# Optimization experiments

Measured on AMD Instinct MI355X. Metric: run time of the kernel, lower is better.

## Reference

```python
import jax, jax.numpy as jnp
import numpy as np

N, E, DIM, A = 100_000, 1_600_000, 128, 5
ODE_STEPS = 5


def setup_inputs() -> dict:
    key = jax.random.key(0)
    ks = jax.random.split(key, 10)
    s = np.float32(1.0 / np.sqrt(DIM))
    s2 = np.float32(1.0 / np.sqrt(2 * DIM))
    return dict(
        x=jax.random.normal(ks[0], (N, DIM), jnp.float32),
        edge_index=jax.random.randint(ks[1], (2, E), 0, N, dtype=jnp.int32),
        node_anchor=jax.random.normal(ks[2], (A, DIM), jnp.float32) * s,
        W_att=jax.random.normal(ks[3], (A, DIM), jnp.float32) * s,
        b_att=jnp.zeros((A,), jnp.float32),
        edge_anchor=jax.random.normal(ks[4], (A, DIM), jnp.float32) * s,
        W_edge=jax.random.normal(ks[5], (A, 2 * DIM), jnp.float32) * s2,
        b_edge=jnp.zeros((A,), jnp.float32),
        W1=jax.random.normal(ks[6], (DIM, 2 * DIM), jnp.float32) * s2,
        b1=jnp.zeros((DIM,), jnp.float32),
        W2=jax.random.normal(ks[7], (DIM, DIM), jnp.float32) * s,
        b2=jnp.zeros((DIM,), jnp.float32),
    )


def reference(x, edge_index, node_anchor, W_att, b_att, edge_anchor,
              W_edge, b_edge, W1, b1, W2, b2):
    src, dst = edge_index[0], edge_index[1]

    # NodePromptplus.add: attention-weighted anchor prompt added to x
    att = jax.nn.softmax(x @ W_att.T + b_att, axis=1)          # [N, A]
    node_x = x + att @ node_anchor                             # [N, DIM]

    # EdgePromptplus.get_prompt: per-edge prompt from endpoint features
    combined_x = jnp.concatenate([x[src], x[dst]], axis=1)     # [E, 2*DIM]
    b = jax.nn.softmax(jax.nn.leaky_relu(combined_x @ W_edge.T + b_edge), axis=1)  # [E, A]
    edge_prompt = b @ edge_anchor                              # [E, DIM]

    # index_add_ scatter to both endpoints
    agg = jnp.zeros_like(x).at[src].add(edge_prompt).at[dst].add(edge_prompt)

    # Euler ODE integration: dx = W2 @ relu(W1 @ [evolved, agg])
    dt = jnp.float32(1.0 / ODE_STEPS)
    W1a, W1b = W1[:, :DIM], W1[:, DIM:]
    agg_proj = agg @ W1b.T + b1   # constant across steps; hoisted out of loop
    ev = node_x
    for _ in range(ODE_STEPS):
        h = jax.nn.relu(ev @ W1a.T + agg_proj)
        ev = ev + dt * (h @ W2.T + b2)
    return ev, edge_prompt
```

## Files before the change

kernel.cpp:

```cpp
#include <hip/hip_runtime.h>

#define NN 100000
#define NE 1600000
#define DIM 128
#define NA 5
#define STEPS 5

#define CSCALE3 128.0f
#define CINV3   0.0078125f

typedef float f32x4 __attribute__((ext_vector_type(4)));
typedef short short8v __attribute__((ext_vector_type(8)));
typedef unsigned u32x4 __attribute__((ext_vector_type(4)));

__device__ __forceinline__ float wsum(float v) {
#pragma unroll
  for (int off = 32; off > 0; off >>= 1) v += __shfl_xor(v, off, 64);
  return v;
}

__device__ __forceinline__ unsigned pkhi(float a, float b) {
  return __builtin_amdgcn_perm(__float_as_uint(b), __float_as_uint(a),
                               0x07060302u);
}
__device__ __forceinline__ float lof(float x) {
  return x - __uint_as_float(__float_as_uint(x) & 0xffff0000u);
}
__device__ __forceinline__ float upk0(unsigned u) {
  return __uint_as_float(u << 16);
}
__device__ __forceinline__ float upk1(unsigned u) {
  return __uint_as_float(u & 0xffff0000u);
}

__global__ __launch_bounds__(128) void k_prepM(
    const float* __restrict__ W1, const float* __restrict__ edge_anchor,
    float* __restrict__ M) {
  const int i = threadIdx.x;
  const int a = blockIdx.x;
  float s = 0.f;
  for (int j = 0; j < DIM; ++j)
    s = fmaf(edge_anchor[a * DIM + j], W1[i * 2 * DIM + DIM + j], s);
  M[a * DIM + i] = s;
}

__global__ __launch_bounds__(256) void k_wpack(
    const float* __restrict__ W1, const float* __restrict__ W2,
    uint4* __restrict__ wp) {
  const int mat = blockIdx.x >> 3, nf = blockIdx.x & 7;
  const int ks = threadIdx.x >> 6, lane = threadIdx.x & 63;
  const int g = lane >> 4, r = lane & 15;
  float v[8];
  if (mat == 0) {
    const float* src = W1 + (16 * nf + r) * 256 + 32 * ks + 8 * g;
    float4 a = *(const float4*)src;
    float4 b = *(const float4*)(src + 4);
    v[0] = a.x; v[1] = a.y; v[2] = a.z; v[3] = a.w;
    v[4] = b.x; v[5] = b.y; v[6] = b.z; v[7] = b.w;
  } else {
    const int trow = 32 * (nf >> 1) + 8 * (r >> 2) + 4 * (nf & 1) + (r & 3);
    const float* src = W2 + trow * 128 + 32 * ks + 4 * g;
    float4 a = *(const float4*)src;
    float4 b = *(const float4*)(src + 16);
    v[0] = a.x; v[1] = a.y; v[2] = a.z; v[3] = a.w;
    v[4] = b.x; v[5] = b.y; v[6] = b.z; v[7] = b.w;
  }
  unsigned h[4], l[4];
#pragma unroll
  for (int w = 0; w < 4; ++w) {
    h[w] = pkhi(v[2 * w], v[2 * w + 1]);
    l[w] = pkhi(lof(v[2 * w]), lof(v[2 * w + 1]));
  }
  wp[((mat * 2 + 0) * 32 + nf * 4 + ks) * 64 + lane] =
      make_uint4(h[0], h[1], h[2], h[3]);
  wp[((mat * 2 + 1) * 32 + nf * 4 + ks) * 64 + lane] =
      make_uint4(l[0], l[1], l[2], l[3]);
}

__global__ __launch_bounds__(256) void k_node(
    const float* __restrict__ x, const float* __restrict__ W_att,
    const float* __restrict__ b_att, const float* __restrict__ node_anchor,
    const float* __restrict__ W_edge, const float* __restrict__ b_edge,
    float* __restrict__ node_x, float* __restrict__ p12) {
  const int wid = threadIdx.x >> 6, lane = threadIdx.x & 63;
  const int d0 = lane << 1;
  float wa0[NA], wa1[NA], we10[NA], we11[NA], we20[NA], we21[NA];
  float na0[NA], na1[NA], ba[NA], be[NA];
#pragma unroll
  for (int a = 0; a < NA; ++a) {
    wa0[a] = W_att[a * DIM + d0];
    wa1[a] = W_att[a * DIM + d0 + 1];
    we10[a] = W_edge[a * 2 * DIM + d0];
    we11[a] = W_edge[a * 2 * DIM + d0 + 1];
    we20[a] = W_edge[a * 2 * DIM + DIM + d0];
    we21[a] = W_edge[a * 2 * DIM + DIM + d0 + 1];
    na0[a] = node_anchor[a * DIM + d0];
    na1[a] = node_anchor[a * DIM + d0 + 1];
    ba[a] = b_att[a];
    be[a] = b_edge[a];
  }
  const int stride = gridDim.x << 2;
  for (int n = (blockIdx.x << 2) + wid; n < NN; n += stride) {
    float2 xv = *(const float2*)(x + (size_t)n * DIM + d0);
    float att[NA], p1[NA], p2[NA];
#pragma unroll
    for (int a = 0; a < NA; ++a) {
      att[a] = wsum(xv.x * wa0[a] + xv.y * wa1[a]) + ba[a];
      p1[a] = wsum(xv.x * we10[a] + xv.y * we11[a]) + be[a];
      p2[a] = wsum(xv.x * we20[a] + xv.y * we21[a]);
    }
    float m = fmaxf(fmaxf(fmaxf(att[0], att[1]), fmaxf(att[2], att[3])), att[4]);
    float s = 0.f;
#pragma unroll
    for (int a = 0; a < NA; ++a) { att[a] = expf(att[a] - m); s += att[a]; }
    float inv = 1.f / s;
    float2 nx = xv;
#pragma unroll
    for (int a = 0; a < NA; ++a) {
      float w = att[a] * inv;
      nx.x = fmaf(w, na0[a], nx.x);
      nx.y = fmaf(w, na1[a], nx.y);
    }
    *(float2*)(node_x + (size_t)n * DIM + d0) = nx;
    if (lane < NA) {
      float v1 = p1[0], v2 = p2[0];
#pragma unroll
      for (int a = 1; a < NA; ++a)
        if (lane == a) { v1 = p1[a]; v2 = p2[a]; }
      p12[(size_t)n * 12 + lane] = v1;
      p12[(size_t)n * 12 + 6 + lane] = v2;
    }
  }
}

__device__ __forceinline__ void edge_b(const float* __restrict__ p12, int src,
                                       int dst, float* __restrict__ b) {
  float4 q1 = *(const float4*)(p12 + (size_t)src * 12);
  float p14 = p12[(size_t)src * 12 + 4];
  float2 r0 = *(const float2*)(p12 + (size_t)dst * 12 + 6);
  float2 r1 = *(const float2*)(p12 + (size_t)dst * 12 + 8);
  float p24 = p12[(size_t)dst * 12 + 10];
  float l[NA] = {q1.x + r0.x, q1.y + r0.y, q1.z + r1.x, q1.w + r1.y,
                 p14 + p24};
#pragma unroll
  for (int a = 0; a < NA; ++a) l[a] = l[a] >= 0.f ? l[a] : 0.01f * l[a];
  float m = fmaxf(fmaxf(fmaxf(l[0], l[1]), fmaxf(l[2], l[3])), l[4]);
  float s = 0.f;
#pragma unroll
  for (int a = 0; a < NA; ++a) { l[a] = expf(l[a] - m); s += l[a]; }
  float inv = 1.f / s;
#pragma unroll
  for (int a = 0; a < NA; ++a) b[a] = l[a] * inv;
}

__global__ __launch_bounds__(256) void k_edge2(
    const int* __restrict__ ei, const float* __restrict__ p12,
    const float* __restrict__ edge_anchor,
    unsigned long long* __restrict__ coeffp, float* __restrict__ ep) {
  __shared__ float bs[4][64][8];
  const int t = threadIdx.x;
  const int w = t >> 6, lane = t & 63;
  const int e = blockIdx.x * 256 + t;
  {
    const int src = ei[e], dst = ei[NE + e];
    float b[NA];
    edge_b(p12, src, dst, b);
    unsigned long long q0 = (unsigned)fmaf(b[0], CSCALE3, 0.5f);
    unsigned long long q1 = (unsigned)fmaf(b[1], CSCALE3, 0.5f);
    unsigned long long q2 = (unsigned)fmaf(b[2], CSCALE3, 0.5f);
    unsigned long long q3 = (unsigned)fmaf(b[3], CSCALE3, 0.5f);
    unsigned long long wv =
        q0 | (q1 << 14) | (q2 << 28) | (q3 << 42) | (1ull << 56);
    atomicAdd(coeffp + src, wv);
    atomicAdd(coeffp + dst, wv);
    *(float4*)&bs[w][lane][0] = make_float4(b[0], b[1], b[2], b[3]);
    bs[w][lane][4] = b[4];
  }
  const int esub = lane >> 5, d0 = (lane & 31) << 2;
  float4 ea4[NA];
#pragma unroll
  for (int a = 0; a < NA; ++a)
    ea4[a] = *(const float4*)(edge_anchor + a * DIM + d0);
  const size_t ebase = (size_t)blockIdx.x * 256 + ((size_t)w << 6);
#pragma unroll 2
  for (int k = 0; k < 32; ++k) {
    const int el = 2 * k + esub;
    float4 c = *(const float4*)&bs[w][el][0];
    float c4 = bs[w][el][4];
    f32x4 v;
#pragma unroll
    for (int i = 0; i < 4; ++i) {
      float s = c.x * ((const float*)&ea4[0])[i];
      s = fmaf(c.y, ((const float*)&ea4[1])[i], s);
      s = fmaf(c.z, ((const float*)&ea4[2])[i], s);
      s = fmaf(c.w, ((const float*)&ea4[3])[i], s);
      s = fmaf(c4, ((const float*)&ea4[4])[i], s);
      v[i] = s;
    }
    __builtin_nontemporal_store(v, (f32x4*)(ep + (ebase + el) * DIM + d0));
  }
}

#define WF(MAT, PART, IDX) (*(const short8v*)&wl[MAT][PART][IDX][lane])

#define MFMA3(WH, WO, BH, BL, ACC)                                            \
  ACC = __builtin_amdgcn_mfma_f32_16x16x32_bf16(                              \
      WH, __builtin_bit_cast(short8v, BH), ACC, 0, 0, 0);                     \
  ACC = __builtin_amdgcn_mfma_f32_16x16x32_bf16(                              \
      WH, __builtin_bit_cast(short8v, BL), ACC, 0, 0, 0);                     \
  ACC = __builtin_amdgcn_mfma_f32_16x16x32_bf16(                              \
      WO, __builtin_bit_cast(short8v, BH), ACC, 0, 0, 0);

#define LOADKS(KS, BH, BL)                                                    \
  {                                                                           \
    float4 a = make_float4(0.f, 0.f, 0.f, 0.f), b = a;                        \
    if (ok) {                                                                 \
      const float* p = ev + (size_t)node * DIM + 32 * KS + 8 * g;             \
      a = *(const float4*)p;                                                  \
      b = *(const float4*)(p + 4);                                            \
    }                                                                         \
    BH[0] = pkhi(a.x, a.y); BL[0] = pkhi(lof(a.x), lof(a.y));                 \
    BH[1] = pkhi(a.z, a.w); BL[1] = pkhi(lof(a.z), lof(a.w));                 \
    BH[2] = pkhi(b.x, b.y); BL[2] = pkhi(lof(b.x), lof(b.y));                 \
    BH[3] = pkhi(b.z, b.w); BL[3] = pkhi(lof(b.z), lof(b.w));                 \
  }

#define MV1NF(NF, QH, QL, W0)                                                 \
  {                                                                           \
    float4 bb = *(const float4*)&b1s[16 * NF + 4 * g];                        \
    f32x4 acc = {bb.x, bb.y, bb.z, bb.w};                                     \
    {                                                                         \
      float4 mm = *(const float4*)&Ms[0][16 * NF + 4 * g];                    \
      acc[0] = fmaf(c0, mm.x, acc[0]); acc[1] = fmaf(c0, mm.y, acc[1]);       \
      acc[2] = fmaf(c0, mm.z, acc[2]); acc[3] = fmaf(c0, mm.w, acc[3]);       \
    }                                                                         \
    {                                                                         \
      float4 mm = *(const float4*)&Ms[1][16 * NF + 4 * g];                    \
      acc[0] = fmaf(c1, mm.x, acc[0]); acc[1] = fmaf(c1, mm.y, acc[1]);       \
      acc[2] = fmaf(c1, mm.z, acc[2]); acc[3] = fmaf(c1, mm.w, acc[3]);       \
    }                                                                         \
    {                                                                         \
      float4 mm = *(const float4*)&Ms[2][16 * NF + 4 * g];                    \
      acc[0] = fmaf(c2, mm.x, acc[0]); acc[1] = fmaf(c2, mm.y, acc[1]);       \
      acc[2] = fmaf(c2, mm.z, acc[2]); acc[3] = fmaf(c2, mm.w, acc[3]);       \
    }                                                                         \
    {                                                                         \
      float4 mm = *(const float4*)&Ms[3][16 * NF + 4 * g];                    \
      acc[0] = fmaf(c3, mm.x, acc[0]); acc[1] = fmaf(c3, mm.y, acc[1]);       \
      acc[2] = fmaf(c3, mm.z, acc[2]); acc[3] = fmaf(c3, mm.w, acc[3]);       \
    }                                                                         \
    {                                                                         \
      float4 mm = *(const float4*)&Ms[4][16 * NF + 4 * g];                    \
      acc[0] = fmaf(c4, mm.x, acc[0]); acc[1] = fmaf(c4, mm.y, acc[1]);       \
      acc[2] = fmaf(c4, mm.z, acc[2]); acc[3] = fmaf(c4, mm.w, acc[3]);       \
    }                                                                         \
    f32x4 accB = {0.f, 0.f, 0.f, 0.f};                                        \
    { short8v wh = WF(0, 0, NF * 4 + 0), wo = WF(0, 1, NF * 4 + 0);           \
      MFMA3(wh, wo, Bh0, Bl0, acc) }                                          \
    { short8v wh = WF(0, 0, NF * 4 + 1), wo = WF(0, 1, NF * 4 + 1);           \
      MFMA3(wh, wo, Bh1, Bl1, accB) }                                         \
    { short8v wh = WF(0, 0, NF * 4 + 2), wo = WF(0, 1, NF * 4 + 2);           \
      MFMA3(wh, wo, Bh2, Bl2, acc) }                                          \
    { short8v wh = WF(0, 0, NF * 4 + 3), wo = WF(0, 1, NF * 4 + 3);           \
      MFMA3(wh, wo, Bh3, Bl3, accB) }                                         \
    float h0 = fmaxf(acc[0] + accB[0], 0.f);                                  \
    float h1 = fmaxf(acc[1] + accB[1], 0.f);                                  \
    float h2 = fmaxf(acc[2] + accB[2], 0.f);                                  \
    float h3 = fmaxf(acc[3] + accB[3], 0.f);                                  \
    QH[W0] = pkhi(h0, h1);                                                    \
    QH[W0 + 1] = pkhi(h2, h3);                                                \
    QL[W0] = pkhi(lof(h0), lof(h1));                                          \
    QL[W0 + 1] = pkhi(lof(h2), lof(h3));                                      \
  }

#define MV2KQ(KQ, BH, BL)                                                     \
  {                                                                           \
    f32x4 a2a = {0.f, 0.f, 0.f, 0.f}, a2aB = a2a;                             \
    { short8v wh = WF(1, 0, (2 * KQ) * 4 + 0), wo = WF(1, 1, (2 * KQ) * 4 + 0); \
      MFMA3(wh, wo, Qh0, Ql0, a2a) }                                          \
    { short8v wh = WF(1, 0, (2 * KQ) * 4 + 1), wo = WF(1, 1, (2 * KQ) * 4 + 1); \
      MFMA3(wh, wo, Qh1, Ql1, a2aB) }                                         \
    { short8v wh = WF(1, 0, (2 * KQ) * 4 + 2), wo = WF(1, 1, (2 * KQ) * 4 + 2); \
      MFMA3(wh, wo, Qh2, Ql2, a2a) }                                          \
    { short8v wh = WF(1, 0, (2 * KQ) * 4 + 3), wo = WF(1, 1, (2 * KQ) * 4 + 3); \
      MFMA3(wh, wo, Qh3, Ql3, a2aB) }                                         \
    f32x4 a2b = {0.f, 0.f, 0.f, 0.f}, a2bB = a2b;                             \
    { short8v wh = WF(1, 0, (2 * KQ + 1) * 4 + 0), wo = WF(1, 1, (2 * KQ + 1) * 4 + 0); \
      MFMA3(wh, wo, Qh0, Ql0, a2b) }                                          \
    { short8v wh = WF(1, 0, (2 * KQ + 1) * 4 + 1), wo = WF(1, 1, (2 * KQ + 1) * 4 + 1); \
      MFMA3(wh, wo, Qh1, Ql1, a2bB) }                                         \
    { short8v wh = WF(1, 0, (2 * KQ + 1) * 4 + 2), wo = WF(1, 1, (2 * KQ + 1) * 4 + 2); \
      MFMA3(wh, wo, Qh2, Ql2, a2b) }                                          \
    { short8v wh = WF(1, 0, (2 * KQ + 1) * 4 + 3), wo = WF(1, 1, (2 * KQ + 1) * 4 + 3); \
      MFMA3(wh, wo, Qh3, Ql3, a2bB) }                                         \
    if (ok) {                                                                 \
      float4 bv0 = *(const float4*)&b2s[32 * KQ + 8 * g];                     \
      float4 bv1 = *(const float4*)&b2s[32 * KQ + 8 * g + 4];                 \
      float4 o0, o1;                                                          \
      o0.x = upk0(BH[0]) + upk0(BL[0]) + fmaf(dt, a2a[0] + a2aB[0], bv0.x);   \
      o0.y = upk1(BH[0]) + upk1(BL[0]) + fmaf(dt, a2a[1] + a2aB[1], bv0.y);   \
      o0.z = upk0(BH[1]) + upk0(BL[1]) + fmaf(dt, a2a[2] + a2aB[2], bv0.z);   \
      o0.w = upk1(BH[1]) + upk1(BL[1]) + fmaf(dt, a2a[3] + a2aB[3], bv0.w);   \
      o1.x = upk0(BH[2]) + upk0(BL[2]) + fmaf(dt, a2b[0] + a2bB[0], bv1.x);   \
      o1.y = upk1(BH[2]) + upk1(BL[2]) + fmaf(dt, a2b[1] + a2bB[1], bv1.y);   \
      o1.z = upk0(BH[3]) + upk0(BL[3]) + fmaf(dt, a2b[2] + a2bB[2], bv1.z);   \
      o1.w = upk1(BH[3]) + upk1(BL[3]) + fmaf(dt, a2b[3] + a2bB[3], bv1.w);   \
      float* p = ev + (size_t)node * DIM + 32 * KQ + 8 * g;                   \
      *(float4*)p = o0;                                                       \
      *(float4*)(p + 4) = o1;                                                 \
    }                                                                         \
  }

__global__ __launch_bounds__(512) void k_step(
    const unsigned long long* __restrict__ coeffp, const float* __restrict__ M,
    const uint4* __restrict__ wp, const float* __restrict__ b1,
    const float* __restrict__ b2, float* __restrict__ ev) {
  __shared__ uint4 wl[2][2][32][64];
  __shared__ float b2s[DIM];
  __shared__ float b1s[DIM];
  __shared__ float Ms[NA][DIM];
  const int tid = threadIdx.x;
  {
    uint4* dst = &wl[0][0][0][0];
#pragma unroll
    for (int i = 0; i < 16; ++i) dst[i * 512 + tid] = wp[i * 512 + tid];
  }
  if (tid < DIM) {
    b2s[tid] = (1.f / STEPS) * b2[tid];
    b1s[tid] = b1[tid];
  }
  if (tid >= DIM && tid < DIM + NA * DIM / 4) {
    const int q = tid - DIM;
    ((float4*)&Ms[0][0])[q] = ((const float4*)M)[q];
  }
  const int wid = tid >> 6, lane = tid & 63;
  const int g = lane >> 4, r = lane & 15;
  const int node = blockIdx.x * 128 + wid * 16 + r;
  const bool ok = node < NN;
  const float dt = 1.f / STEPS;

  u32x4 Bh0, Bh1, Bh2, Bh3, Bl0, Bl1, Bl2, Bl3;
  LOADKS(0, Bh0, Bl0)
  LOADKS(1, Bh1, Bl1)
  LOADKS(2, Bh2, Bl2)
  LOADKS(3, Bh3, Bl3)

  float c0 = 0.f, c1 = 0.f, c2 = 0.f, c3 = 0.f, c4 = 0.f;
  if (ok) {
    unsigned long long v = coeffp[node];
    c0 = (float)(unsigned)(v & 0x3FFFu) * CINV3;
    c1 = (float)(unsigned)((v >> 14) & 0x3FFFu) * CINV3;
    c2 = (float)(unsigned)((v >> 28) & 0x3FFFu) * CINV3;
    c3 = (float)(unsigned)((v >> 42) & 0x3FFFu) * CINV3;
    float cnt = (float)(unsigned)(v >> 56);
    c4 = cnt - (c0 + c1 + c2 + c3);
  }
  __syncthreads();

  u32x4 Qh0, Qh1, Qh2, Qh3, Ql0, Ql1, Ql2, Ql3;
  MV1NF(0, Qh0, Ql0, 0)
  MV1NF(1, Qh0, Ql0, 2)
  MV1NF(2, Qh1, Ql1, 0)
  MV1NF(3, Qh1, Ql1, 2)
  MV1NF(4, Qh2, Ql2, 0)
  MV1NF(5, Qh2, Ql2, 2)
  MV1NF(6, Qh3, Ql3, 0)
  MV1NF(7, Qh3, Ql3, 2)
  MV2KQ(0, Bh0, Bl0)
  MV2KQ(1, Bh1, Bl1)
  MV2KQ(2, Bh2, Bl2)
  MV2KQ(3, Bh3, Bl3)
}

extern "C" void kernel_launch(void* const* d_in, const int* in_sizes, int n_in,
                              void* d_out, int out_size, void* d_ws,
                              size_t ws_size, hipStream_t stream) {
  const float* x = (const float*)d_in[0];
  const int* ei = (const int*)d_in[1];
  const float* node_anchor = (const float*)d_in[2];
  const float* W_att = (const float*)d_in[3];
  const float* b_att = (const float*)d_in[4];
  const float* edge_anchor = (const float*)d_in[5];
  const float* W_edge = (const float*)d_in[6];
  const float* b_edge = (const float*)d_in[7];
  const float* W1 = (const float*)d_in[8];
  const float* b1 = (const float*)d_in[9];
  const float* W2 = (const float*)d_in[10];
  const float* b2 = (const float*)d_in[11];

  float* out = (float*)d_out;
  float* ev = out;
  float* ep = out + (size_t)NN * DIM;

  char* ws = (char*)d_ws;
  float* p12 = (float*)(ws);
  unsigned long long* coeffp =
      (unsigned long long*)(ws + 4800000);
  float* Mm = (float*)(ws + 5600000);
  uint4* wpack = (uint4*)(ws + 5602560);

  hipMemsetAsync(coeffp, 0, (size_t)NN * sizeof(unsigned long long), stream);
  k_prepM<<<NA, DIM, 0, stream>>>(W1, edge_anchor, Mm);
  k_wpack<<<16, 256, 0, stream>>>(W1, W2, wpack);
  k_node<<<2048, 256, 0, stream>>>(x, W_att, b_att, node_anchor, W_edge, b_edge,
                                   ev, p12);
  k_edge2<<<NE / 256, 256, 0, stream>>>(ei, p12, edge_anchor, coeffp, ep);
  for (int s = 0; s < STEPS; ++s)
    k_step<<<(NN + 127) / 128, 512, 0, stream>>>(coeffp, Mm, wpack, b1, b2, ev);
}
```

Measured before the change: 510.7 us.

## Fuse two ODE Euler steps per kernel, keeping state in registers

Adds k_step2, which runs two Euler steps back to back. The intermediate evolved state stays in registers as packed hi/lo bf16 pairs and is never written to global memory. The launch sequence becomes two k_step2 calls plus one k_step, replacing five k_step launches. This is meant to save the global read/write of ev, the weight staging into shared memory, and the per-launch overhead between steps. In exchange it adds register pressure and code size.

```diff
diff --git a/kernel.cpp b/kernel.cpp
--- a/kernel.cpp
+++ b/kernel.cpp
@@ -273,26 +273,29 @@
     QL[W0 + 1] = pkhi(lof(h2), lof(h3));                                      \
   }
 
+#define MV2CORE(KQ)                                                           \
+  f32x4 a2a = {0.f, 0.f, 0.f, 0.f}, a2aB = a2a;                               \
+  { short8v wh = WF(1, 0, (2 * KQ) * 4 + 0), wo = WF(1, 1, (2 * KQ) * 4 + 0); \
+    MFMA3(wh, wo, Qh0, Ql0, a2a) }                                            \
+  { short8v wh = WF(1, 0, (2 * KQ) * 4 + 1), wo = WF(1, 1, (2 * KQ) * 4 + 1); \
+    MFMA3(wh, wo, Qh1, Ql1, a2aB) }                                           \
+  { short8v wh = WF(1, 0, (2 * KQ) * 4 + 2), wo = WF(1, 1, (2 * KQ) * 4 + 2); \
+    MFMA3(wh, wo, Qh2, Ql2, a2a) }                                            \
+  { short8v wh = WF(1, 0, (2 * KQ) * 4 + 3), wo = WF(1, 1, (2 * KQ) * 4 + 3); \
+    MFMA3(wh, wo, Qh3, Ql3, a2aB) }                                           \
+  f32x4 a2b = {0.f, 0.f, 0.f, 0.f}, a2bB = a2b;                               \
+  { short8v wh = WF(1, 0, (2 * KQ + 1) * 4 + 0), wo = WF(1, 1, (2 * KQ + 1) * 4 + 0); \
+    MFMA3(wh, wo, Qh0, Ql0, a2b) }                                            \
+  { short8v wh = WF(1, 0, (2 * KQ + 1) * 4 + 1), wo = WF(1, 1, (2 * KQ + 1) * 4 + 1); \
+    MFMA3(wh, wo, Qh1, Ql1, a2bB) }                                           \
+  { short8v wh = WF(1, 0, (2 * KQ + 1) * 4 + 2), wo = WF(1, 1, (2 * KQ + 1) * 4 + 2); \
+    MFMA3(wh, wo, Qh2, Ql2, a2b) }                                            \
+  { short8v wh = WF(1, 0, (2 * KQ + 1) * 4 + 3), wo = WF(1, 1, (2 * KQ + 1) * 4 + 3); \
+    MFMA3(wh, wo, Qh3, Ql3, a2bB) }
+
 #define MV2KQ(KQ, BH, BL)                                                     \
   {                                                                           \
-    f32x4 a2a = {0.f, 0.f, 0.f, 0.f}, a2aB = a2a;                             \
-    { short8v wh = WF(1, 0, (2 * KQ) * 4 + 0), wo = WF(1, 1, (2 * KQ) * 4 + 0); \
-      MFMA3(wh, wo, Qh0, Ql0, a2a) }                                          \
-    { short8v wh = WF(1, 0, (2 * KQ) * 4 + 1), wo = WF(1, 1, (2 * KQ) * 4 + 1); \
-      MFMA3(wh, wo, Qh1, Ql1, a2aB) }                                         \
-    { short8v wh = WF(1, 0, (2 * KQ) * 4 + 2), wo = WF(1, 1, (2 * KQ) * 4 + 2); \
-      MFMA3(wh, wo, Qh2, Ql2, a2a) }                                          \
-    { short8v wh = WF(1, 0, (2 * KQ) * 4 + 3), wo = WF(1, 1, (2 * KQ) * 4 + 3); \
-      MFMA3(wh, wo, Qh3, Ql3, a2aB) }                                         \
-    f32x4 a2b = {0.f, 0.f, 0.f, 0.f}, a2bB = a2b;                             \
-    { short8v wh = WF(1, 0, (2 * KQ + 1) * 4 + 0), wo = WF(1, 1, (2 * KQ + 1) * 4 + 0); \
-      MFMA3(wh, wo, Qh0, Ql0, a2b) }                                          \
-    { short8v wh = WF(1, 0, (2 * KQ + 1) * 4 + 1), wo = WF(1, 1, (2 * KQ + 1) * 4 + 1); \
-      MFMA3(wh, wo, Qh1, Ql1, a2bB) }                                         \
-    { short8v wh = WF(1, 0, (2 * KQ + 1) * 4 + 2), wo = WF(1, 1, (2 * KQ + 1) * 4 + 2); \
-      MFMA3(wh, wo, Qh2, Ql2, a2b) }                                          \
-    { short8v wh = WF(1, 0, (2 * KQ + 1) * 4 + 3), wo = WF(1, 1, (2 * KQ + 1) * 4 + 3); \
-      MFMA3(wh, wo, Qh3, Ql3, a2bB) }                                         \
+    MV2CORE(KQ)                                                               \
     if (ok) {                                                                 \
       float4 bv0 = *(const float4*)&b2s[32 * KQ + 8 * g];                     \
       float4 bv1 = *(const float4*)&b2s[32 * KQ + 8 * g + 4];                 \
@@ -311,65 +314,108 @@
     }                                                                         \
   }
 
+#define MV2KQR(KQ, BH, BL)                                                    \
+  {                                                                           \
+    MV2CORE(KQ)                                                               \
+    float4 bv0 = *(const float4*)&b2s[32 * KQ + 8 * g];                       \
+    float4 bv1 = *(const float4*)&b2s[32 * KQ + 8 * g + 4];                   \
+    float n0 = upk0(BH[0]) + upk0(BL[0]) + fmaf(dt, a2a[0] + a2aB[0], bv0.x); \
+    float n1 = upk1(BH[0]) + upk1(BL[0]) + fmaf(dt, a2a[1] + a2aB[1], bv0.y); \
+    float n2 = upk0(BH[1]) + upk0(BL[1]) + fmaf(dt, a2a[2] + a2aB[2], bv0.z); \
+    float n3 = upk1(BH[1]) + upk1(BL[1]) + fmaf(dt, a2a[3] + a2aB[3], bv0.w); \
+    float n4 = upk0(BH[2]) + upk0(BL[2]) + fmaf(dt, a2b[0] + a2bB[0], bv1.x); \
+    float n5 = upk1(BH[2]) + upk1(BL[2]) + fmaf(dt, a2b[1] + a2bB[1], bv1.y); \
+    float n6 = upk0(BH[3]) + upk0(BL[3]) + fmaf(dt, a2b[2] + a2bB[2], bv1.z); \
+    float n7 = upk1(BH[3]) + upk1(BL[3]) + fmaf(dt, a2b[3] + a2bB[3], bv1.w); \
+    BH[0] = pkhi(n0, n1); BL[0] = pkhi(lof(n0), lof(n1));                     \
+    BH[1] = pkhi(n2, n3); BL[1] = pkhi(lof(n2), lof(n3));                     \
+    BH[2] = pkhi(n4, n5); BL[2] = pkhi(lof(n4), lof(n5));                     \
+    BH[3] = pkhi(n6, n7); BL[3] = pkhi(lof(n6), lof(n7));                     \
+  }
+
+#define MV1_ALL                                                               \
+  MV1NF(0, Qh0, Ql0, 0) MV1NF(1, Qh0, Ql0, 2)                                 \
+  MV1NF(2, Qh1, Ql1, 0) MV1NF(3, Qh1, Ql1, 2)                                 \
+  MV1NF(4, Qh2, Ql2, 0) MV1NF(5, Qh2, Ql2, 2)                                 \
+  MV1NF(6, Qh3, Ql3, 0) MV1NF(7, Qh3, Ql3, 2)
+
+#define PROLOGUE                                                              \
+  __shared__ uint4 wl[2][2][32][64];                                          \
+  __shared__ float b2s[DIM];                                                  \
+  __shared__ float b1s[DIM];                                                  \
+  __shared__ float Ms[NA][DIM];                                               \
+  const int tid = threadIdx.x;                                                \
+  {                                                                           \
+    uint4* dst = &wl[0][0][0][0];                                             \
+    _Pragma("unroll")                                                         \
+    for (int i = 0; i < 16; ++i) dst[i * 512 + tid] = wp[i * 512 + tid];      \
+  }                                                                           \
+  if (tid < DIM) {                                                            \
+    b2s[tid] = (1.f / STEPS) * b2[tid];                                       \
+    b1s[tid] = b1[tid];                                                       \
+  }                                                                           \
+  if (tid >= DIM && tid < DIM + NA * DIM / 4) {                               \
+    const int q = tid - DIM;                                                  \
+    ((float4*)&Ms[0][0])[q] = ((const float4*)M)[q];                          \
+  }                                                                           \
+  const int wid = tid >> 6, lane = tid & 63;                                  \
+  const int g = lane >> 4, r = lane & 15;                                     \
+  const int node = blockIdx.x * 128 + wid * 16 + r;                           \
+  const bool ok = node < NN;                                                  \
+  const float dt = 1.f / STEPS;                                               \
+  u32x4 Bh0, Bh1, Bh2, Bh3, Bl0, Bl1, Bl2, Bl3;                               \
+  LOADKS(0, Bh0, Bl0)                                                         \
+  LOADKS(1, Bh1, Bl1)                                                         \
+  LOADKS(2, Bh2, Bl2)                                                         \
+  LOADKS(3, Bh3, Bl3)                                                         \
+  float c0 = 0.f, c1 = 0.f, c2 = 0.f, c3 = 0.f, c4 = 0.f;                     \
+  if (ok) {                                                                   \
+    unsigned long long v = coeffp[node];                                      \
+    c0 = (float)(unsigned)(v & 0x3FFFu) * CINV3;                              \
+    c1 = (float)(unsigned)((v >> 14) & 0x3FFFu) * CINV3;                      \
+    c2 = (float)(unsigned)((v >> 28) & 0x3FFFu) * CINV3;                      \
+    c3 = (float)(unsigned)((v >> 42) & 0x3FFFu) * CINV3;                      \
+    float cnt = (float)(unsigned)(v >> 56);                                   \
+    c4 = cnt - (c0 + c1 + c2 + c3);                                           \
+  }                                                                           \
+  __syncthreads();
+
 __global__ __launch_bounds__(512) void k_step(
     const unsigned long long* __restrict__ coeffp, const float* __restrict__ M,
     const uint4* __restrict__ wp, const float* __restrict__ b1,
     const float* __restrict__ b2, float* __restrict__ ev) {
-  __shared__ uint4 wl[2][2][32][64];
-  __shared__ float b2s[DIM];
-  __shared__ float b1s[DIM];
-  __shared__ float Ms[NA][DIM];
-  const int tid = threadIdx.x;
-  {
-    uint4* dst = &wl[0][0][0][0];
-#pragma unroll
-    for (int i = 0; i < 16; ++i) dst[i * 512 + tid] = wp[i * 512 + tid];
-  }
-  if (tid < DIM) {
-    b2s[tid] = (1.f / STEPS) * b2[tid];
-    b1s[tid] = b1[tid];
-  }
-  if (tid >= DIM && tid < DIM + NA * DIM / 4) {
-    const int q = tid - DIM;
-    ((float4*)&Ms[0][0])[q] = ((const float4*)M)[q];
-  }
-  const int wid = tid >> 6, lane = tid & 63;
-  const int g = lane >> 4, r = lane & 15;
-  const int node = blockIdx.x * 128 + wid * 16 + r;
-  const bool ok = node < NN;
-  const float dt = 1.f / STEPS;
-
-  u32x4 Bh0, Bh1, Bh2, Bh3, Bl0, Bl1, Bl2, Bl3;
-  LOADKS(0, Bh0, Bl0)
-  LOADKS(1, Bh1, Bl1)
-  LOADKS(2, Bh2, Bl2)
-  LOADKS(3, Bh3, Bl3)
-
-  float c0 = 0.f, c1 = 0.f, c2 = 0.f, c3 = 0.f, c4 = 0.f;
-  if (ok) {
-    unsigned long long v = coeffp[node];
-    c0 = (float)(unsigned)(v & 0x3FFFu) * CINV3;
-    c1 = (float)(unsigned)((v >> 14) & 0x3FFFu) * CINV3;
-    c2 = (float)(unsigned)((v >> 28) & 0x3FFFu) * CINV3;
-    c3 = (float)(unsigned)((v >> 42) & 0x3FFFu) * CINV3;
-    float cnt = (float)(unsigned)(v >> 56);
-    c4 = cnt - (c0 + c1 + c2 + c3);
-  }
-  __syncthreads();
-
+  PROLOGUE
   u32x4 Qh0, Qh1, Qh2, Qh3, Ql0, Ql1, Ql2, Ql3;
-  MV1NF(0, Qh0, Ql0, 0)
-  MV1NF(1, Qh0, Ql0, 2)
-  MV1NF(2, Qh1, Ql1, 0)
-  MV1NF(3, Qh1, Ql1, 2)
-  MV1NF(4, Qh2, Ql2, 0)
-  MV1NF(5, Qh2, Ql2, 2)
-  MV1NF(6, Qh3, Ql3, 0)
-  MV1NF(7, Qh3, Ql3, 2)
+  MV1_ALL
   MV2KQ(0, Bh0, Bl0)
   MV2KQ(1, Bh1, Bl1)
   MV2KQ(2, Bh2, Bl2)
   MV2KQ(3, Bh3, Bl3)
+}
+
+__global__ __launch_bounds__(512) void k_step2(
+    const unsigned long long* __restrict__ coeffp, const float* __restrict__ M,
+    const uint4* __restrict__ wp, const float* __restrict__ b1,
+    const float* __restrict__ b2, float* __restrict__ ev) {
+  PROLOGUE
+  {
+    u32x4 Qh0, Qh1, Qh2, Qh3, Ql0, Ql1, Ql2, Ql3;
+    MV1_ALL
+    MV2KQR(0, Bh0, Bl0)
+    MV2KQR(1, Bh1, Bl1)
+    MV2KQR(2, Bh2, Bl2)
+    MV2KQR(3, Bh3, Bl3)
+  }
+  __syncthreads();
+  __builtin_amdgcn_sched_barrier(0);
+  {
+    u32x4 Qh0, Qh1, Qh2, Qh3, Ql0, Ql1, Ql2, Ql3;
+    MV1_ALL
+    MV2KQ(0, Bh0, Bl0)
+    MV2KQ(1, Bh1, Bl1)
+    MV2KQ(2, Bh2, Bl2)
+    MV2KQ(3, Bh3, Bl3)
+  }
 }
 
 extern "C" void kernel_launch(void* const* d_in, const int* in_sizes, int n_in,
@@ -405,6 +451,8 @@
   k_node<<<2048, 256, 0, stream>>>(x, W_att, b_att, node_anchor, W_edge, b_edge,
                                    ev, p12);
   k_edge2<<<NE / 256, 256, 0, stream>>>(ei, p12, edge_anchor, coeffp, ep);
-  for (int s = 0; s < STEPS; ++s)
-    k_step<<<(NN + 127) / 128, 512, 0, stream>>>(coeffp, Mm, wpack, b1, b2, ev);
-}
+  const int nb = (NN + 127) / 128;
+  k_step2<<<nb, 512, 0, stream>>>(coeffp, Mm, wpack, b1, b2, ev);
+  k_step2<<<nb, 512, 0, stream>>>(coeffp, Mm, wpack, b1, b2, ev);
+  k_step<<<nb, 512, 0, stream>>>(coeffp, Mm, wpack, b1, b2, ev);
+}
```

Result: faster. 466.9 us (-8.6%).
